# Kernel optimization log

Measured on AMD Instinct MI355X. Metric: run time of the kernel, lower is better.

## Reference

```python
import jax, jax.numpy as jnp
import numpy as np

N = 200_000   # num_nodes
E = 100_000   # events per direction
D = 128       # memory_dim
F = 128       # event feature dim
T = 128       # time encoding dim


def setup_inputs() -> dict:
    key = jax.random.key(0)
    ks = jax.random.split(key, 12)
    src = jax.random.randint(ks[0], (E,), 0, N)
    dst = jax.random.randint(ks[1], (E,), 0, N)
    t = jax.random.uniform(ks[2], (E,)) * 1000.0
    feat = jax.random.normal(ks[3], (E, F))
    memory = jax.random.normal(ks[4], (N, D)) * 0.1
    last_update = jnp.zeros((N,), dtype=jnp.float32)
    time_w = jax.random.normal(ks[5], (T,)) * 0.1
    time_b = jax.random.normal(ks[6], (T,)) * 0.1
    M = 2 * D + T + F  # message dim = 512
    w_ih = jax.random.normal(ks[7], (3 * D, M)) * 0.02
    w_hh = jax.random.normal(ks[8], (3 * D, D)) * 0.02
    b_ih = jnp.zeros((3 * D,), dtype=jnp.float32)
    b_hh = jnp.zeros((3 * D,), dtype=jnp.float32)
    return {
        "memory": memory, "last_update": last_update, "t": t, "feat": feat,
        "time_w": time_w, "time_b": time_b,
        "w_ih": w_ih, "w_hh": w_hh, "b_ih": b_ih, "b_hh": b_hh,
        "src": src, "dst": dst,
    }


def time_encode(dt, w, b):
    # TGN/TGAT-style cosine time encoding: [E] -> [E, T]
    return jnp.cos(dt[:, None] * w[None, :] + b[None, :])


def gru_cell(x, h, w_ih, w_hh, b_ih, b_hh):
    # Standard torch.nn.GRUCell math (gates ordered r, z, n).
    gi = x @ w_ih.T + b_ih  # [N, 3D]
    gh = h @ w_hh.T + b_hh  # [N, 3D]
    i_r, i_z, i_n = jnp.split(gi, 3, axis=-1)
    h_r, h_z, h_n = jnp.split(gh, 3, axis=-1)
    r = jax.nn.sigmoid(i_r + h_r)
    z = jax.nn.sigmoid(i_z + h_z)
    n = jnp.tanh(i_n + r * h_n)
    return (1.0 - z) * n + z * h


def reference(memory, last_update, t, feat, time_w, time_b,
              w_ih, w_hh, b_ih, b_hh, src, dst):
    # --- message functions (identity = concat), both directions ---
    s_msg = jnp.concatenate(
        [memory[src], memory[dst], time_encode(t - last_update[src], time_w, time_b), feat], axis=-1)
    d_msg = jnp.concatenate(
        [memory[dst], memory[src], time_encode(t - last_update[dst], time_w, time_b), feat], axis=-1)

    nodes = jnp.concatenate([src, dst], axis=0)        # [2E]
    te = jnp.concatenate([t, t], axis=0)               # [2E]
    msg = jnp.concatenate([s_msg, d_msg], axis=0)      # [2E, M]

    # --- 'last' aggregator: per-node argmax over event time (scatter_max) ---
    # Stable sort by time; segment_max over sorted positions yields, per node,
    # the latest event (ties broken toward the later original index).
    perm = jnp.argsort(te, stable=True)                # [2E]
    pos = jnp.arange(2 * E)
    best_pos = jax.ops.segment_max(pos, nodes[perm], num_segments=N)  # [N], intmin if empty
    has_msg = best_pos >= 0
    best = perm[jnp.clip(best_pos, 0)]                 # [N] event index of latest msg

    agg_msg = msg[best]                                # [N, M] gather
    max_t = te[best]                                   # [N]

    # --- GRU memory update + masked scatter back into memory ---
    new_mem = gru_cell(agg_msg, memory, w_ih, w_hh, b_ih, b_hh)
    new_memory = jnp.where(has_msg[:, None], new_mem, memory)
    new_last_update = jnp.where(has_msg, max_t, last_update)
    return new_memory, new_last_update
```

## Files before the change

### kernel.cpp

```cpp
#include <hip/hip_runtime.h>
#include <hip/hip_bf16.h>
#include <stdint.h>

typedef __hip_bfloat16 bf16;
typedef unsigned long long u64;
typedef unsigned int u32;
typedef short short8 __attribute__((ext_vector_type(8)));
typedef float f32x4 __attribute__((ext_vector_type(4)));

#define D_ 128
#define BM 64
#define BN 128
#define BK 64
#define KFB 640
#define BM2 32

__device__ __forceinline__ float bf2f(bf16 v) { return __bfloat162float(v); }
__device__ __forceinline__ u32 fbits(float f) { union { float f; u32 u; } c; c.f = f; return c.u; }
__device__ __forceinline__ u32 pk2(float a, float b) {
  union { bf16 h; unsigned short s; } x, y;
  x.h = __float2bfloat16(a); y.h = __float2bfloat16(b);
  return (u32)x.s | ((u32)y.s << 16);
}
template<bool F32>
__device__ __forceinline__ float ldE(const void* p, size_t i) {
  return F32 ? ((const float*)p)[i] : bf2f(((const bf16*)p)[i]);
}
template<bool F32>
__device__ __forceinline__ void stE(void* p, size_t i, float v) {
  if (F32) ((float*)p)[i] = v; else ((bf16*)p)[i] = __float2bfloat16(v);
}
template<bool F32>
__device__ __forceinline__ uint4 ld8(const void* base, size_t elemOff) {
  if (!F32) {
    return *(const uint4*)((const bf16*)base + elemOff);
  } else {
    const float4* p = (const float4*)((const float*)base + elemOff);
    float4 v0 = p[0], v1 = p[1];
    uint4 o; o.x = pk2(v0.x, v0.y); o.y = pk2(v0.z, v0.w);
    o.z = pk2(v1.x, v1.y); o.w = pk2(v1.z, v1.w);
    return o;
  }
}
template<bool F32>
__device__ __forceinline__ void stage8(const void* base, size_t elemOff, bf16* dst) {
  *(uint4*)dst = ld8<F32>(base, elemOff);
}
__device__ __forceinline__ void gl_lds16(const void* g, void* l) {
  __builtin_amdgcn_global_load_lds(
      (const __attribute__((address_space(1))) unsigned int*)g,
      (__attribute__((address_space(3))) unsigned int*)l, 16, 0, 0);
}

__global__ void k_prep(u64* __restrict__ key, u32* __restrict__ cnt, int N,
                       const u32* __restrict__ mem_w, const u32* __restrict__ t_w,
                       u32* __restrict__ flag) {
  int i = blockIdx.x * blockDim.x + threadIdx.x;
  if (i < N) key[i] = 0ull;
  if (i == 0) {
    *cnt = 0u;
    int ok = 1;
    for (int k = 0; k < 64; ++k) {
      u32 w = mem_w[k];
      if ((w & 0x7fffu) > 0x4300u) ok = 0;
      if (((w >> 16) & 0x7fffu) > 0x4300u) ok = 0;
    }
    for (int k = 0; k < 16; ++k) {
      u32 w = t_w[k];
      if ((w & 0xffffu) > 0x4480u) ok = 0;
      if ((w >> 16) > 0x4480u) ok = 0;
    }
    *flag = ok ? 0u : 1u;
  }
}

__global__ void k_scat(const int* __restrict__ src, const int* __restrict__ dst,
                       const void* __restrict__ t, const u32* __restrict__ flag,
                       u64* __restrict__ key, int E) {
  int i = blockIdx.x * blockDim.x + threadIdx.x;
  if (i >= 2 * E) return;
  int e = (i < E) ? i : i - E;
  int node = (i < E) ? src[e] : dst[e];
  float tv = (*flag) ? ((const float*)t)[e] : bf2f(((const bf16*)t)[e]);
  u64 k = ((u64)fbits(tv) << 32) | (u64)(u32)(i + 1);
  atomicMax(&key[node], k);
}

__global__ void k_pack2(const void* __restrict__ wih, const void* __restrict__ whh,
                        const u32* __restrict__ flag, bf16* __restrict__ wpk) {
  int gid = blockIdx.x * 256 + threadIdx.x;
  if (gid >= 32768) return;
  int tile = gid >> 10, r = gid & 1023;
  int j = r >> 3, s = r & 7;
  int kc = tile >> 2, by = tile & 3;
  int kglob = kc * 64 + s * 8;
  int grp = j >> 5, gi = j & 31, gidx = 32 * by + gi;
  bool F = (*flag != 0);
  float f[8];
#pragma unroll
  for (int q = 0; q < 8; ++q) {
    int k = kglob + q;
    float v = 0.f;
    if (grp < 3) {
      int srow = grp * 128 + gidx;
      v = F ? ldE<true>(wih, (size_t)srow * 512 + k) : ldE<false>(wih, (size_t)srow * 512 + k);
      if (k < 128 && grp < 2)
        v += F ? ldE<true>(whh, (size_t)srow * 128 + k) : ldE<false>(whh, (size_t)srow * 128 + k);
    } else if (k < 128) {
      v = F ? ldE<true>(whh, (size_t)(256 + gidx) * 128 + k)
            : ldE<false>(whh, (size_t)(256 + gidx) * 128 + k);
    }
    f[q] = v;
  }
  uint4 o; o.x = pk2(f[0], f[1]); o.y = pk2(f[2], f[3]);
  o.z = pk2(f[4], f[5]); o.w = pk2(f[6], f[7]);
  ((uint4*)wpk)[(size_t)tile * 1024 + ((j * 8 + s) ^ (j & 7))] = o;
}

template<bool F32>
__device__ __forceinline__ void compact_body(int n, bool nvalid,
                                             const void* mem, const void* lastup,
                                             const void* t, const u64* key,
                                             int* list, u32* cnt, int use_list,
                                             void* out, int N, int E, u32* s_wb) {
  u32 b = 0;
  if (nvalid) b = (u32)key[n];
  bool active = nvalid && (b != 0u);
  if (use_list) {
    u64 mask = __ballot(active);
    int lane = threadIdx.x & 63, w = threadIdx.x >> 6;
    if (lane == 0) s_wb[w] = (u32)__popcll(mask);
    __syncthreads();
    if (threadIdx.x == 0) {
      u32 tot = s_wb[0] + s_wb[1] + s_wb[2] + s_wb[3];
      u32 base = tot ? atomicAdd(cnt, tot) : 0u;
      u32 acc0 = base;
      for (int i = 0; i < 4; ++i) { u32 c = s_wb[i]; s_wb[i] = acc0; acc0 += c; }
    }
    __syncthreads();
    if (active) {
      u32 idx = s_wb[w] + (u32)__popcll(mask & ((1ull << lane) - 1ull));
      list[idx] = n;
    }
  }
  if (!nvalid) return;
  if (active) {
    int pos = (int)(b - 1u);
    int e = (pos < E) ? pos : pos - E;
    stE<F32>(out, (size_t)N * D_ + n, ldE<F32>(t, e));
  } else {
    if (F32) {
      const float4* s = (const float4*)((const float*)mem + (size_t)n * D_);
      float4* d = (float4*)((float*)out + (size_t)n * D_);
#pragma unroll
      for (int i = 0; i < 32; ++i) d[i] = s[i];
    } else {
      const uint4* s = (const uint4*)((const bf16*)mem + (size_t)n * D_);
      uint4* d = (uint4*)((bf16*)out + (size_t)n * D_);
#pragma unroll
      for (int i = 0; i < 16; ++i) d[i] = s[i];
    }
    stE<F32>(out, (size_t)N * D_ + n, ldE<F32>(lastup, n));
  }
}
__global__ void k_compact(const void* mem, const void* lastup, const void* t,
                          const u32* __restrict__ flag, const u64* __restrict__ key,
                          int* list, u32* cnt, int use_list,
                          void* out, int N, int E) {
  __shared__ u32 s_wb[4];
  int n = blockIdx.x * blockDim.x + threadIdx.x;
  bool nvalid = (n < N);
  if (*flag) compact_body<true>(n, nvalid, mem, lastup, t, key, list, cnt, use_list, out, N, E, s_wb);
  else       compact_body<false>(n, nvalid, mem, lastup, t, key, list, cnt, use_list, out, N, E, s_wb);
}

template<bool F32>
__device__ __forceinline__ uint4 a_fetch(int kcn, int tid,
    const void* mem, const void* feat,
    const int* s_node, const int* s_e, const int* s_oth,
    const float* s_dt, const float* s_tw, const float* s_tb) {
  int r = tid >> 3, s = tid & 7;
  int k0 = kcn * 64 + s * 8;
  if (k0 < 128) return ld8<F32>(mem, (size_t)s_node[r] * D_ + k0);
  if (k0 < 256) return ld8<F32>(mem, (size_t)s_oth[r] * D_ + (k0 - 128));
  if (k0 < 384) {
    float dtv = s_dt[r];
    float f[8];
#pragma unroll
    for (int q = 0; q < 8; ++q) {
      int j = k0 - 256 + q;
      f[q] = cosf(fmaf(dtv, s_tw[j], s_tb[j]));
    }
    uint4 o; o.x = pk2(f[0], f[1]); o.y = pk2(f[2], f[3]);
    o.z = pk2(f[4], f[5]); o.w = pk2(f[6], f[7]);
    return o;
  }
  return ld8<F32>(feat, (size_t)s_e[r] * D_ + (k0 - 384));
}

__device__ __forceinline__ void b_issue(const bf16* __restrict__ wpk, int tile,
                                        bf16* BsBuf, int tid) {
  int w = tid >> 6;
  const bf16* g = wpk + (size_t)tile * 8192 + w * 2048 + (tid & 63) * 8;
  bf16* l = BsBuf + w * 2048;
#pragma unroll
  for (int i = 0; i < 4; ++i)
    gl_lds16(g + i * 512, l + i * 512);
}

template<bool F32>
__device__ __forceinline__ void gemm2_body(
    const void* mem, const void* lastup, const void* t, const void* feat,
    const int* __restrict__ src, const int* __restrict__ dst,
    const bf16* __restrict__ wpk,
    const void* bih, const void* bhh, const void* tw, const void* tb,
    const u64* __restrict__ key, const int* __restrict__ list,
    const u32* __restrict__ cnt, int use_list,
    void* out, int N, int E,
    char* smem, int* s_node, int* s_e, int* s_oth, int* s_act,
    float* s_dt, float* s_tw, float* s_tb) {
  const int tid = threadIdx.x;
  const int bx = blockIdx.x;
  bf16 (*As)[BM2][72] = (bf16 (*)[BM2][72])smem;
  bf16* BsBase = (bf16*)(smem + 9216);
  float (*Gs)[133] = (float (*)[133])smem;

  b_issue(wpk, 0, BsBase, tid);

  if (tid < BM2) {
    int r = tid, row = BM2 * bx + r, node = -1;
    if (use_list) { int c = (int)*cnt; if (row < c) node = list[row]; }
    else if (row < N) node = row;
    int act = 0, e = 0, oth = 0; float dtv = 0.f;
    if (node >= 0) {
      u32 b = (u32)key[node];
      if (b) {
        act = 1;
        int pos = (int)(b - 1u);
        if (pos < E) { e = pos; oth = dst[e]; } else { e = pos - E; oth = src[e]; }
        dtv = ldE<F32>(t, e) - ldE<F32>(lastup, node);
      }
    }
    if (node < 0) node = 0;
    s_node[r] = node; s_e[r] = e; s_oth[r] = oth; s_act[r] = act; s_dt[r] = dtv;
  }
  if (tid < 128) s_tw[tid] = ldE<F32>(tw, tid);
  else           s_tb[tid - 128] = ldE<F32>(tb, tid - 128);
  __syncthreads();

  {
    uint4 a0 = a_fetch<F32>(0, tid, mem, feat, s_node, s_e, s_oth, s_dt, s_tw, s_tb);
    *(uint4*)&As[0][tid >> 3][(tid & 7) * 8] = a0;
  }
  __syncthreads();

  const int w = tid >> 6, l = tid & 63;
  const int mrow = l & 15, quad = l >> 4;
  const bool w3 = (w == 3);
  f32x4 acc[4][2][2];
#pragma unroll
  for (int by = 0; by < 4; ++by)
#pragma unroll
    for (int mi = 0; mi < 2; ++mi)
#pragma unroll
      for (int ni = 0; ni < 2; ++ni) acc[by][mi][ni] = (f32x4){0.f, 0.f, 0.f, 0.f};

  uint4 apre = (uint4){0u, 0u, 0u, 0u};
#pragma unroll 1
  for (int kc = 0; kc < 8; ++kc) {
    const int ka = kc & 1;
    short8 a[2][2];
#pragma unroll
    for (int by = 0; by < 4; ++by) {
      const int tile = kc * 4 + by;
      if (by == 0) {
        if (kc + 1 < 8)
          apre = a_fetch<F32>(kc + 1, tid, mem, feat, s_node, s_e, s_oth, s_dt, s_tw, s_tb);
      }
      if (tile + 1 < 32 && !(w3 && (tile + 1) >= 8))
        b_issue(wpk, tile + 1, BsBase + (((by & 1) ^ 1) << 13), tid);
      if (by == 0) {
#pragma unroll
        for (int ks2 = 0; ks2 < 2; ++ks2)
#pragma unroll
          for (int mi = 0; mi < 2; ++mi)
            a[ks2][mi] = *(const short8*)((const char*)&As[ka][0][0] +
                             (16 * mi + mrow) * 144 + ks2 * 64 + quad * 16);
      }
      if (!(w3 && kc >= 2)) {
        const char* Bsb = (const char*)(BsBase + ((by & 1) << 13));
        short8 b[2][2];
#pragma unroll
        for (int ks2 = 0; ks2 < 2; ++ks2)
#pragma unroll
          for (int ni = 0; ni < 2; ++ni) {
            int j = 32 * w + 16 * ni + mrow;
            int off = (j * 128 + ks2 * 64 + quad * 16) ^ ((j & 7) << 4);
            b[ks2][ni] = *(const short8*)(Bsb + off);
          }
        __builtin_amdgcn_s_setprio(1);
#pragma unroll
        for (int ks2 = 0; ks2 < 2; ++ks2)
#pragma unroll
          for (int mi = 0; mi < 2; ++mi)
#pragma unroll
            for (int ni = 0; ni < 2; ++ni)
              acc[by][mi][ni] = __builtin_amdgcn_mfma_f32_16x16x32_bf16(
                  a[ks2][mi], b[ks2][ni], acc[by][mi][ni], 0, 0, 0);
        __builtin_amdgcn_s_setprio(0);
      }
      if (by == 3 && kc + 1 < 8)
        *(uint4*)&As[ka ^ 1][tid >> 3][(tid & 7) * 8] = apre;
      __syncthreads();
    }
  }

#pragma unroll
  for (int by = 0; by < 4; ++by) {
#pragma unroll
    for (int mi = 0; mi < 2; ++mi)
#pragma unroll
      for (int ni = 0; ni < 2; ++ni)
#pragma unroll
        for (int reg = 0; reg < 4; ++reg)
          Gs[16 * mi + quad * 4 + reg][32 * w + 16 * ni + mrow] = acc[by][mi][ni][reg];
    __syncthreads();
    {
      int r = tid >> 3, giB = (tid & 7) * 4;
      if (s_act[r]) {
        int node = s_node[r];
#pragma unroll
        for (int q = 0; q < 4; ++q) {
          int gi = giB + q, gidx = 32 * by + gi;
          float rp  = Gs[r][gi]      + ldE<F32>(bih, gidx)       + ldE<F32>(bhh, gidx);
          float zp  = Gs[r][32 + gi] + ldE<F32>(bih, 128 + gidx) + ldE<F32>(bhh, 128 + gidx);
          float inp = Gs[r][64 + gi] + ldE<F32>(bih, 256 + gidx);
          float hnp = Gs[r][96 + gi] + ldE<F32>(bhh, 256 + gidx);
          float rg = 1.f / (1.f + expf(-rp));
          float zg = 1.f / (1.f + expf(-zp));
          float ng = tanhf(inp + rg * hnp);
          float h = ldE<F32>(mem, (size_t)node * D_ + gidx);
          stE<F32>(out, (size_t)node * D_ + gidx, (1.f - zg) * ng + zg * h);
        }
      }
    }
    __syncthreads();
  }
}

__global__ __launch_bounds__(256, 3)
void k_gemm2(const void* mem, const void* lastup, const void* t, const void* feat,
             const int* src, const int* dst, const bf16* wpk,
             const void* bih, const void* bhh, const void* tw, const void* tb,
             const u32* __restrict__ flag, const u64* __restrict__ key,
             const int* __restrict__ list, const u32* __restrict__ cnt, int use_list,
             void* out, int N, int E) {
  if (use_list && (int)*cnt <= BM2 * (int)blockIdx.x) return;
  __shared__ __align__(16) char smem[41984];
  __shared__ int s_node[BM2], s_e[BM2], s_oth[BM2], s_act[BM2];
  __shared__ float s_dt[BM2], s_tw[128], s_tb[128];
  if (*flag)
    gemm2_body<true>(mem, lastup, t, feat, src, dst, wpk, bih, bhh, tw, tb,
                     key, list, cnt, use_list, out, N, E,
                     smem, s_node, s_e, s_oth, s_act, s_dt, s_tw, s_tb);
  else
    gemm2_body<false>(mem, lastup, t, feat, src, dst, wpk, bih, bhh, tw, tb,
                      key, list, cnt, use_list, out, N, E,
                      smem, s_node, s_e, s_oth, s_act, s_dt, s_tw, s_tb);
}

template<bool F32>
__device__ __forceinline__ void gemm_body(
    const void* mem, const void* lastup, const void* t, const void* feat,
    const int* __restrict__ src, const int* __restrict__ dst,
    const void* wih, const void* whh, const void* bih, const void* bhh,
    const void* tw, const void* tb,
    const u64* __restrict__ key, const int* __restrict__ list,
    const u32* __restrict__ cnt, int use_list,
    void* out, int N, int E,
    bf16 (*As)[72], bf16 (*Bs)[72], float (*Gs)[132],
    int* s_node, int* s_e, int* s_oth, int* s_act, float* s_dt) {
  const int tid = threadIdx.x;
  const int bx = blockIdx.x, by = blockIdx.y;

  if (tid < BM) {
    int r = tid;
    int row = BM * bx + r;
    int node = -1;
    if (use_list) { int c = (int)*cnt; if (row < c) node = list[row]; }
    else if (row < N) node = row;
    int act = 0, e = 0, oth = 0; float dtv = 0.f;
    if (node >= 0) {
      u32 b = (u32)key[node];
      if (b) {
        act = 1;
        int pos = (int)(b - 1u);
        if (pos < E) { e = pos; oth = dst[e]; } else { e = pos - E; oth = src[e]; }
        dtv = ldE<F32>(t, e) - ldE<F32>(lastup, node);
      }
    }
    if (node < 0) node = 0;
    s_node[r] = node; s_e[r] = e; s_oth[r] = oth; s_act[r] = act; s_dt[r] = dtv;
  }

  const int w = tid >> 6, l = tid & 63;
  const int mrow = l & 15, quad = l >> 4;
  f32x4 acc[4][2];
#pragma unroll
  for (int mi = 0; mi < 4; ++mi)
#pragma unroll
    for (int ni = 0; ni < 2; ++ni) acc[mi][ni] = (f32x4){0.f, 0.f, 0.f, 0.f};

#pragma unroll 1
  for (int kc = 0; kc < KFB / BK; ++kc) {
    __syncthreads();
#pragma unroll
    for (int it = 0; it < 2; ++it) {
      int task = tid + 256 * it;
      int r = task >> 3, s = task & 7;
      int k0 = kc * BK + s * 8;
      bf16* dstp = &As[r][s * 8];
      if (k0 < 128)       stage8<F32>(mem,  (size_t)s_node[r] * D_ + k0, dstp);
      else if (k0 < 256)  stage8<F32>(mem,  (size_t)s_oth[r] * D_ + (k0 - 128), dstp);
      else if (k0 < 384) {
        float dtv = s_dt[r];
        float f[8];
#pragma unroll
        for (int q = 0; q < 8; ++q) {
          int j = k0 - 256 + q;
          f[q] = cosf(fmaf(dtv, ldE<F32>(tw, j), ldE<F32>(tb, j)));
        }
        uint4 o; o.x = pk2(f[0], f[1]); o.y = pk2(f[2], f[3]);
        o.z = pk2(f[4], f[5]); o.w = pk2(f[6], f[7]);
        *(uint4*)dstp = o;
      }
      else if (k0 < 512)  stage8<F32>(feat, (size_t)s_e[r] * D_ + (k0 - 384), dstp);
      else                stage8<F32>(mem,  (size_t)s_node[r] * D_ + (k0 - 512), dstp);
    }
#pragma unroll
    for (int it = 0; it < 4; ++it) {
      int task = tid + 256 * it;
      int j = task >> 3, s = task & 7;
      int k0 = kc * BK + s * 8;
      int grp = j >> 5, gi = j & 31;
      int gidx = 32 * by + gi;
      bf16* dstp = &Bs[j][s * 8];
      if (k0 < 512) {
        if (grp == 3) { *(uint4*)dstp = (uint4){0, 0, 0, 0}; }
        else {
          int srow = (grp == 0) ? gidx : (grp == 1) ? 128 + gidx : 256 + gidx;
          stage8<F32>(wih, (size_t)srow * 512 + k0, dstp);
        }
      } else {
        if (grp == 2) { *(uint4*)dstp = (uint4){0, 0, 0, 0}; }
        else {
          int srow = (grp == 0) ? gidx : (grp == 1) ? 128 + gidx : 256 + gidx;
          stage8<F32>(whh, (size_t)srow * D_ + (k0 - 512), dstp);
        }
      }
    }
    __syncthreads();
#pragma unroll
    for (int ks = 0; ks < BK; ks += 32) {
      short8 a[4], b[2];
#pragma unroll
      for (int mi = 0; mi < 4; ++mi)
        a[mi] = *(const short8*)&As[16 * mi + mrow][ks + quad * 8];
#pragma unroll
      for (int ni = 0; ni < 2; ++ni)
        b[ni] = *(const short8*)&Bs[32 * w + 16 * ni + mrow][ks + quad * 8];
#pragma unroll
      for (int mi = 0; mi < 4; ++mi)
#pragma unroll
        for (int ni = 0; ni < 2; ++ni)
          acc[mi][ni] = __builtin_amdgcn_mfma_f32_16x16x32_bf16(a[mi], b[ni], acc[mi][ni], 0, 0, 0);
    }
  }

#pragma unroll
  for (int mi = 0; mi < 4; ++mi)
#pragma unroll
    for (int ni = 0; ni < 2; ++ni)
#pragma unroll
      for (int reg = 0; reg < 4; ++reg)
        Gs[16 * mi + quad * 4 + reg][32 * w + 16 * ni + mrow] = acc[mi][ni][reg];
  __syncthreads();

  {
    int r = tid >> 2;
    int giB = (tid & 3) * 8;
    if (s_act[r]) {
      int node = s_node[r];
#pragma unroll
      for (int q = 0; q < 8; ++q) {
        int gi = giB + q;
        int gidx = 32 * by + gi;
        float rp  = Gs[r][gi]       + ldE<F32>(bih, gidx)       + ldE<F32>(bhh, gidx);
        float zp  = Gs[r][32 + gi]  + ldE<F32>(bih, 128 + gidx) + ldE<F32>(bhh, 128 + gidx);
        float inp = Gs[r][64 + gi]  + ldE<F32>(bih, 256 + gidx);
        float hnp = Gs[r][96 + gi]  + ldE<F32>(bhh, 256 + gidx);
        float rg = 1.f / (1.f + expf(-rp));
        float zg = 1.f / (1.f + expf(-zp));
        float ng = tanhf(inp + rg * hnp);
        float h = ldE<F32>(mem, (size_t)node * D_ + gidx);
        stE<F32>(out, (size_t)node * D_ + gidx, (1.f - zg) * ng + zg * h);
      }
    }
  }
}

__global__ __launch_bounds__(256)
void k_gemm_fb(const void* mem, const void* lastup, const void* t, const void* feat,
               const int* src, const int* dst,
               const void* wih, const void* whh, const void* bih, const void* bhh,
               const void* tw, const void* tb,
               const u32* __restrict__ flag, const u64* __restrict__ key,
               const int* __restrict__ list, const u32* __restrict__ cnt, int use_list,
               void* out, int N, int E) {
  if (use_list && (int)*cnt <= BM * (int)blockIdx.x) return;

  __shared__ __align__(16) bf16 As[BM][72];
  __shared__ __align__(16) bf16 Bs[BN][72];
  __shared__ __align__(16) float Gs[BM][132];
  __shared__ int s_node[BM], s_e[BM], s_oth[BM], s_act[BM];
  __shared__ float s_dt[BM];

  if (*flag)
    gemm_body<true>(mem, lastup, t, feat, src, dst, wih, whh, bih, bhh, tw, tb,
                    key, list, cnt, use_list, out, N, E,
                    As, Bs, Gs, s_node, s_e, s_oth, s_act, s_dt);
  else
    gemm_body<false>(mem, lastup, t, feat, src, dst, wih, whh, bih, bhh, tw, tb,
                     key, list, cnt, use_list, out, N, E,
                     As, Bs, Gs, s_node, s_e, s_oth, s_act, s_dt);
}

extern "C" void kernel_launch(void* const* d_in, const int* in_sizes, int n_in,
                              void* d_out, int out_size, void* d_ws, size_t ws_size,
                              hipStream_t stream) {
  const void* mem    = d_in[0];
  const void* lastup = d_in[1];
  const void* t      = d_in[2];
  const void* feat   = d_in[3];
  const void* tw     = d_in[4];
  const void* tb     = d_in[5];
  const void* wih    = d_in[6];
  const void* whh    = d_in[7];
  const void* bih    = d_in[8];
  const void* bhh    = d_in[9];
  const int*  src    = (const int*)d_in[10];
  const int*  dst    = (const int*)d_in[11];

  int N = in_sizes[0] / D_;
  int E = in_sizes[2];

  char* ws = (char*)d_ws;
  size_t off = 0;
  u32* flag = (u32*)(ws + off); off += 16;
  u32* cnt  = (u32*)(ws + off); off += 16;
  u64* key  = (u64*)(ws + off); off += (size_t)N * 8;
  int* list = (int*)(ws + off); off += (size_t)N * 4;
  int use_list = (ws_size >= off) ? 1 : 0;
  bf16* wpk = (bf16*)(ws + off); off += (size_t)32 * 8192 * 2;
  int use2 = (ws_size >= off) ? 1 : 0;

  const int thr = 256;
  int nb = (N + thr - 1) / thr;
  int eb = (2 * E + thr - 1) / thr;

  k_prep<<<dim3(nb), dim3(thr), 0, stream>>>(key, cnt, N, (const u32*)mem, (const u32*)t, flag);
  k_scat<<<dim3(eb), dim3(thr), 0, stream>>>(src, dst, t, flag, key, E);
  if (use2)
    k_pack2<<<dim3(128), dim3(thr), 0, stream>>>(wih, whh, flag, wpk);
  k_compact<<<dim3(nb), dim3(thr), 0, stream>>>(mem, lastup, t, flag, key,
                                                list, cnt, use_list, d_out, N, E);
  if (use2) {
    int mt = (N + BM2 - 1) / BM2;
    k_gemm2<<<dim3(mt), dim3(thr), 0, stream>>>(
        mem, lastup, t, feat, src, dst, wpk, bih, bhh, tw, tb,
        flag, key, list, cnt, use_list, d_out, N, E);
  } else {
    int mt = (N + BM - 1) / BM;
    k_gemm_fb<<<dim3(mt, 4), dim3(thr), 0, stream>>>(
        mem, lastup, t, feat, src, dst, wih, whh, bih, bhh, tw, tb,
        flag, key, list, cnt, use_list, d_out, N, E);
  }
}
```

Baseline: 480.2 us.

## Fuse weight packing into prep kernel and deepen B-tile prefetch with vmcnt waits

Merges the weight-packing kernel into the key-reset prep kernel, removing one launch. The GEMM main loop now prefetches B tiles two steps ahead. It replaces per-step __syncthreads with hand-tuned s_waitcnt vmcnt counts plus a single barrier per k-chunk. A-operand global loads are split into a raw fetch and a later bf16 pack, so the conversion happens after the loads land. The hand-counted vmcnt values are fragile. They depend on exact instruction counts per dtype path, and a miscount could read stale LDS data. The warp-3 skip of the gate-n tiles past the hidden width is also dropped, so that wave now does extra MFMAs on zero weights.

```diff
diff --git a/kernel.cpp b/kernel.cpp
--- a/kernel.cpp
+++ b/kernel.cpp
@@ -14,6 +14,8 @@
 #define BK 64
 #define KFB 640
 #define BM2 32
+
+#define VMWAIT(n) asm volatile("s_waitcnt vmcnt(" #n ")" ::: "memory")
 
 __device__ __forceinline__ float bf2f(bf16 v) { return __bfloat162float(v); }
 __device__ __forceinline__ u32 fbits(float f) { union { float f; u32 u; } c; c.f = f; return c.u; }
@@ -52,25 +54,59 @@
       (__attribute__((address_space(3))) unsigned int*)l, 16, 0, 0);
 }
 
-__global__ void k_prep(u64* __restrict__ key, u32* __restrict__ cnt, int N,
-                       const u32* __restrict__ mem_w, const u32* __restrict__ t_w,
-                       u32* __restrict__ flag) {
-  int i = blockIdx.x * blockDim.x + threadIdx.x;
+__device__ __forceinline__ u32 sniff_dtype(const u32* mem_w, const u32* t_w) {
+  int ok = 1;
+  for (int k = 0; k < 64; ++k) {
+    u32 w = mem_w[k];
+    if ((w & 0x7fffu) > 0x4300u) ok = 0;
+    if (((w >> 16) & 0x7fffu) > 0x4300u) ok = 0;
+  }
+  for (int k = 0; k < 16; ++k) {
+    u32 w = t_w[k];
+    if ((w & 0xffffu) > 0x4480u) ok = 0;
+    if ((w >> 16) > 0x4480u) ok = 0;
+  }
+  return ok ? 0u : 1u;
+}
+
+__global__ void k_preppack(u64* __restrict__ key, u32* __restrict__ cnt, int N,
+                           const u32* __restrict__ mem_w, const u32* __restrict__ t_w,
+                           u32* __restrict__ flag,
+                           const void* __restrict__ wih, const void* __restrict__ whh,
+                           bf16* __restrict__ wpk, int do_pack) {
+  __shared__ u32 s_ok;
+  int i = blockIdx.x * 256 + threadIdx.x;
   if (i < N) key[i] = 0ull;
-  if (i == 0) {
-    *cnt = 0u;
-    int ok = 1;
-    for (int k = 0; k < 64; ++k) {
-      u32 w = mem_w[k];
-      if ((w & 0x7fffu) > 0x4300u) ok = 0;
-      if (((w >> 16) & 0x7fffu) > 0x4300u) ok = 0;
-    }
-    for (int k = 0; k < 16; ++k) {
-      u32 w = t_w[k];
-      if ((w & 0xffffu) > 0x4480u) ok = 0;
-      if ((w >> 16) > 0x4480u) ok = 0;
-    }
-    *flag = ok ? 0u : 1u;
+  if (i == 0) { *cnt = 0u; *flag = sniff_dtype(mem_w, t_w); }
+  if (do_pack && blockIdx.x < 128) {
+    if (threadIdx.x == 0) s_ok = sniff_dtype(mem_w, t_w);
+    __syncthreads();
+    bool F = (s_ok != 0);
+    int gid = blockIdx.x * 256 + threadIdx.x;
+    int tile = gid >> 10, r = gid & 1023;
+    int j = r >> 3, s = r & 7;
+    int kc = tile >> 2, by = tile & 3;
+    int kglob = kc * 64 + s * 8;
+    int grp = j >> 5, gi = j & 31, gidx = 32 * by + gi;
+    float f[8];
+#pragma unroll
+    for (int q = 0; q < 8; ++q) {
+      int k = kglob + q;
+      float v = 0.f;
+      if (grp < 3) {
+        int srow = grp * 128 + gidx;
+        v = F ? ldE<true>(wih, (size_t)srow * 512 + k) : ldE<false>(wih, (size_t)srow * 512 + k);
+        if (k < 128 && grp < 2)
+          v += F ? ldE<true>(whh, (size_t)srow * 128 + k) : ldE<false>(whh, (size_t)srow * 128 + k);
+      } else if (k < 128) {
+        v = F ? ldE<true>(whh, (size_t)(256 + gidx) * 128 + k)
+              : ldE<false>(whh, (size_t)(256 + gidx) * 128 + k);
+      }
+      f[q] = v;
+    }
+    uint4 o; o.x = pk2(f[0], f[1]); o.y = pk2(f[2], f[3]);
+    o.z = pk2(f[4], f[5]); o.w = pk2(f[6], f[7]);
+    ((uint4*)wpk)[(size_t)tile * 1024 + ((j * 8 + s) ^ (j & 7))] = o;
   }
 }
 
@@ -84,37 +120,6 @@
   float tv = (*flag) ? ((const float*)t)[e] : bf2f(((const bf16*)t)[e]);
   u64 k = ((u64)fbits(tv) << 32) | (u64)(u32)(i + 1);
   atomicMax(&key[node], k);
-}
-
-__global__ void k_pack2(const void* __restrict__ wih, const void* __restrict__ whh,
-                        const u32* __restrict__ flag, bf16* __restrict__ wpk) {
-  int gid = blockIdx.x * 256 + threadIdx.x;
-  if (gid >= 32768) return;
-  int tile = gid >> 10, r = gid & 1023;
-  int j = r >> 3, s = r & 7;
-  int kc = tile >> 2, by = tile & 3;
-  int kglob = kc * 64 + s * 8;
-  int grp = j >> 5, gi = j & 31, gidx = 32 * by + gi;
-  bool F = (*flag != 0);
-  float f[8];
-#pragma unroll
-  for (int q = 0; q < 8; ++q) {
-    int k = kglob + q;
-    float v = 0.f;
-    if (grp < 3) {
-      int srow = grp * 128 + gidx;
-      v = F ? ldE<true>(wih, (size_t)srow * 512 + k) : ldE<false>(wih, (size_t)srow * 512 + k);
-      if (k < 128 && grp < 2)
-        v += F ? ldE<true>(whh, (size_t)srow * 128 + k) : ldE<false>(whh, (size_t)srow * 128 + k);
-    } else if (k < 128) {
-      v = F ? ldE<true>(whh, (size_t)(256 + gidx) * 128 + k)
-            : ldE<false>(whh, (size_t)(256 + gidx) * 128 + k);
-    }
-    f[q] = v;
-  }
-  uint4 o; o.x = pk2(f[0], f[1]); o.y = pk2(f[2], f[3]);
-  o.z = pk2(f[4], f[5]); o.w = pk2(f[6], f[7]);
-  ((uint4*)wpk)[(size_t)tile * 1024 + ((j * 8 + s) ^ (j & 7))] = o;
 }
 
 template<bool F32>
@@ -174,28 +179,51 @@
   else       compact_body<false>(n, nvalid, mem, lastup, t, key, list, cnt, use_list, out, N, E, s_wb);
 }
 
-template<bool F32>
-__device__ __forceinline__ uint4 a_fetch(int kcn, int tid,
+struct AR { uint4 lo, hi; };
+
+template<bool F32>
+__device__ __forceinline__ AR a_fetch_raw(int kcn, int tid,
     const void* mem, const void* feat,
     const int* s_node, const int* s_e, const int* s_oth,
-    const float* s_dt, const float* s_tw, const float* s_tb) {
+    const float* s_dt, const float* s_twb) {
   int r = tid >> 3, s = tid & 7;
   int k0 = kcn * 64 + s * 8;
-  if (k0 < 128) return ld8<F32>(mem, (size_t)s_node[r] * D_ + k0);
-  if (k0 < 256) return ld8<F32>(mem, (size_t)s_oth[r] * D_ + (k0 - 128));
-  if (k0 < 384) {
+  AR a;
+  if (k0 >= 256 && k0 < 384) {
     float dtv = s_dt[r];
     float f[8];
 #pragma unroll
     for (int q = 0; q < 8; ++q) {
       int j = k0 - 256 + q;
-      f[q] = cosf(fmaf(dtv, s_tw[j], s_tb[j]));
-    }
-    uint4 o; o.x = pk2(f[0], f[1]); o.y = pk2(f[2], f[3]);
-    o.z = pk2(f[4], f[5]); o.w = pk2(f[6], f[7]);
-    return o;
-  }
-  return ld8<F32>(feat, (size_t)s_e[r] * D_ + (k0 - 384));
+      f[q] = cosf(fmaf(dtv, s_twb[j], s_twb[128 + j]));
+    }
+    a.lo.x = pk2(f[0], f[1]); a.lo.y = pk2(f[2], f[3]);
+    a.lo.z = pk2(f[4], f[5]); a.lo.w = pk2(f[6], f[7]);
+    a.hi = a.lo;
+    return a;
+  }
+  const void* base = mem;
+  size_t eo;
+  if (k0 < 128)       eo = (size_t)s_node[r] * D_ + k0;
+  else if (k0 < 256)  eo = (size_t)s_oth[r] * D_ + (k0 - 128);
+  else                { base = feat; eo = (size_t)s_e[r] * D_ + (k0 - 384); }
+  if (F32) {
+    const uint4* p = (const uint4*)((const float*)base + eo);
+    a.lo = p[0]; a.hi = p[1];
+  } else {
+    a.lo = *(const uint4*)((const bf16*)base + eo);
+    a.hi = a.lo;
+  }
+  return a;
+}
+template<bool F32>
+__device__ __forceinline__ uint4 a_pack(AR a, int kcn) {
+  if (!F32) return a.lo;
+  if (kcn == 4 || kcn == 5) return a.lo;
+  union { uint4 u; float4 f; } l, h; l.u = a.lo; h.u = a.hi;
+  uint4 o; o.x = pk2(l.f.x, l.f.y); o.y = pk2(l.f.z, l.f.w);
+  o.z = pk2(h.f.x, h.f.y); o.w = pk2(h.f.z, h.f.w);
+  return o;
 }
 
 __device__ __forceinline__ void b_issue(const bf16* __restrict__ wpk, int tile,
@@ -218,14 +246,12 @@
     const u32* __restrict__ cnt, int use_list,
     void* out, int N, int E,
     char* smem, int* s_node, int* s_e, int* s_oth, int* s_act,
-    float* s_dt, float* s_tw, float* s_tb) {
+    float* s_dt, float* s_twb) {
   const int tid = threadIdx.x;
   const int bx = blockIdx.x;
   bf16 (*As)[BM2][72] = (bf16 (*)[BM2][72])smem;
   bf16* BsBase = (bf16*)(smem + 9216);
   float (*Gs)[133] = (float (*)[133])smem;
-
-  b_issue(wpk, 0, BsBase, tid);
 
   if (tid < BM2) {
     int r = tid, row = BM2 * bx + r, node = -1;
@@ -244,19 +270,21 @@
     if (node < 0) node = 0;
     s_node[r] = node; s_e[r] = e; s_oth[r] = oth; s_act[r] = act; s_dt[r] = dtv;
   }
-  if (tid < 128) s_tw[tid] = ldE<F32>(tw, tid);
-  else           s_tb[tid - 128] = ldE<F32>(tb, tid - 128);
+  if (tid < 128) s_twb[tid] = ldE<F32>(tw, tid);
+  else           s_twb[128 + (tid - 128)] = ldE<F32>(tb, tid - 128);
   __syncthreads();
 
   {
-    uint4 a0 = a_fetch<F32>(0, tid, mem, feat, s_node, s_e, s_oth, s_dt, s_tw, s_tb);
-    *(uint4*)&As[0][tid >> 3][(tid & 7) * 8] = a0;
+    AR a0 = a_fetch_raw<F32>(0, tid, mem, feat, s_node, s_e, s_oth, s_dt, s_twb);
+    *(uint4*)&As[0][tid >> 3][(tid & 7) * 8] = a_pack<F32>(a0, 0);
   }
   __syncthreads();
+
+  b_issue(wpk, 0, BsBase, tid);
+  b_issue(wpk, 1, BsBase + 8192, tid);
 
   const int w = tid >> 6, l = tid & 63;
   const int mrow = l & 15, quad = l >> 4;
-  const bool w3 = (w == 3);
   f32x4 acc[4][2][2];
 #pragma unroll
   for (int by = 0; by < 4; ++by)
@@ -265,20 +293,25 @@
 #pragma unroll
       for (int ni = 0; ni < 2; ++ni) acc[by][mi][ni] = (f32x4){0.f, 0.f, 0.f, 0.f};
 
-  uint4 apre = (uint4){0u, 0u, 0u, 0u};
+  AR apre; apre.lo = (uint4){0,0,0,0}; apre.hi = apre.lo;
 #pragma unroll 1
   for (int kc = 0; kc < 8; ++kc) {
     const int ka = kc & 1;
     short8 a[2][2];
 #pragma unroll
     for (int by = 0; by < 4; ++by) {
-      const int tile = kc * 4 + by;
-      if (by == 0) {
-        if (kc + 1 < 8)
-          apre = a_fetch<F32>(kc + 1, tid, mem, feat, s_node, s_e, s_oth, s_dt, s_tw, s_tb);
-      }
-      if (tile + 1 < 32 && !(w3 && (tile + 1) >= 8))
-        b_issue(wpk, tile + 1, BsBase + (((by & 1) ^ 1) << 13), tid);
+      const int p = 4 * kc + by;
+      if (by == 0 && kc < 7)
+        apre = a_fetch_raw<F32>(kc + 1, tid, mem, feat, s_node, s_e, s_oth, s_dt, s_twb);
+      if (by < 2) {
+        if (kc == 3 || kc == 4 || kc == 7) { VMWAIT(4); }
+        else if (F32)                      { VMWAIT(6); }
+        else                               { VMWAIT(5); }
+      } else if (by == 2)                  { VMWAIT(4); }
+      else {
+        if (kc == 7)                       { VMWAIT(0); }
+        else                               { VMWAIT(4); }
+      }
       if (by == 0) {
 #pragma unroll
         for (int ks2 = 0; ks2 < 2; ++ks2)
@@ -287,31 +320,34 @@
             a[ks2][mi] = *(const short8*)((const char*)&As[ka][0][0] +
                              (16 * mi + mrow) * 144 + ks2 * 64 + quad * 16);
       }
-      if (!(w3 && kc >= 2)) {
-        const char* Bsb = (const char*)(BsBase + ((by & 1) << 13));
-        short8 b[2][2];
-#pragma unroll
-        for (int ks2 = 0; ks2 < 2; ++ks2)
-#pragma unroll
-          for (int ni = 0; ni < 2; ++ni) {
-            int j = 32 * w + 16 * ni + mrow;
-            int off = (j * 128 + ks2 * 64 + quad * 16) ^ ((j & 7) << 4);
-            b[ks2][ni] = *(const short8*)(Bsb + off);
-          }
-        __builtin_amdgcn_s_setprio(1);
-#pragma unroll
-        for (int ks2 = 0; ks2 < 2; ++ks2)
-#pragma unroll
-          for (int mi = 0; mi < 2; ++mi)
-#pragma unroll
-            for (int ni = 0; ni < 2; ++ni)
-              acc[by][mi][ni] = __builtin_amdgcn_mfma_f32_16x16x32_bf16(
-                  a[ks2][mi], b[ks2][ni], acc[by][mi][ni], 0, 0, 0);
-        __builtin_amdgcn_s_setprio(0);
-      }
-      if (by == 3 && kc + 1 < 8)
-        *(uint4*)&As[ka ^ 1][tid >> 3][(tid & 7) * 8] = apre;
-      __syncthreads();
+      const char* Bsb = (const char*)(BsBase + ((p & 1) << 13));
+      short8 b[2][2];
+#pragma unroll
+      for (int ks2 = 0; ks2 < 2; ++ks2)
+#pragma unroll
+        for (int ni = 0; ni < 2; ++ni) {
+          int j = 32 * w + 16 * ni + mrow;
+          int off = (j * 128 + ks2 * 64 + quad * 16) ^ ((j & 7) << 4);
+          b[ks2][ni] = *(const short8*)(Bsb + off);
+        }
+      __builtin_amdgcn_s_setprio(1);
+#pragma unroll
+      for (int ks2 = 0; ks2 < 2; ++ks2)
+#pragma unroll
+        for (int mi = 0; mi < 2; ++mi)
+#pragma unroll
+          for (int ni = 0; ni < 2; ++ni)
+            acc[by][mi][ni] = __builtin_amdgcn_mfma_f32_16x16x32_bf16(
+                a[ks2][mi], b[ks2][ni], acc[by][mi][ni], 0, 0, 0);
+      __builtin_amdgcn_s_setprio(0);
+      if (p + 2 < 32)
+        b_issue(wpk, p + 2, BsBase + ((p & 1) << 13), tid);
+      if (by == 3) {
+        if (kc < 7)
+          *(uint4*)&As[ka ^ 1][tid >> 3][(tid & 7) * 8] = a_pack<F32>(apre, kc + 1);
+        asm volatile("s_waitcnt lgkmcnt(0)" ::: "memory");
+        __builtin_amdgcn_s_barrier();
+      }
     }
   }
 
@@ -358,15 +394,15 @@
   if (use_list && (int)*cnt <= BM2 * (int)blockIdx.x) return;
   __shared__ __align__(16) char smem[41984];
   __shared__ int s_node[BM2], s_e[BM2], s_oth[BM2], s_act[BM2];
-  __shared__ float s_dt[BM2], s_tw[128], s_tb[128];
+  __shared__ float s_dt[BM2], s_twb[256];
   if (*flag)
     gemm2_body<true>(mem, lastup, t, feat, src, dst, wpk, bih, bhh, tw, tb,
                      key, list, cnt, use_list, out, N, E,
-                     smem, s_node, s_e, s_oth, s_act, s_dt, s_tw, s_tb);
+                     smem, s_node, s_e, s_oth, s_act, s_dt, s_twb);
   else
     gemm2_body<false>(mem, lastup, t, feat, src, dst, wpk, bih, bhh, tw, tb,
                       key, list, cnt, use_list, out, N, E,
-                      smem, s_node, s_e, s_oth, s_act, s_dt, s_tw, s_tb);
+                      smem, s_node, s_e, s_oth, s_act, s_dt, s_twb);
 }
 
 template<bool F32>
@@ -568,10 +604,10 @@
   int nb = (N + thr - 1) / thr;
   int eb = (2 * E + thr - 1) / thr;
 
-  k_prep<<<dim3(nb), dim3(thr), 0, stream>>>(key, cnt, N, (const u32*)mem, (const u32*)t, flag);
+  k_preppack<<<dim3(nb), dim3(thr), 0, stream>>>(key, cnt, N, (const u32*)mem,
+                                                 (const u32*)t, flag, wih, whh,
+                                                 wpk, use2);
   k_scat<<<dim3(eb), dim3(thr), 0, stream>>>(src, dst, t, flag, key, E);
-  if (use2)
-    k_pack2<<<dim3(128), dim3(thr), 0, stream>>>(wih, whh, flag, wpk);
   k_compact<<<dim3(nb), dim3(thr), 0, stream>>>(mem, lastup, t, flag, key,
                                                 list, cnt, use_list, d_out, N, E);
   if (use2) {
```

New measurement: 467.9 us. 1.03x faster.
